# Kernel optimization log

Measured on AMD Instinct MI355X. Metric: run time of the kernel, lower is better.

The kernel has to match this reference:

```python
import jax, jax.numpy as jnp
import numpy as np

T = 4        # number of atom types (len(atomtype))
N = 65536    # number of atoms
D = 256      # nl[0] == nl[1] == nl[2]
EPS = 1e-5   # LayerNorm eps (torch default)


def setup_inputs() -> dict:
    key = jax.random.key(0)
    ks = jax.random.split(key, 16)
    s = 1.0 / np.sqrt(D)  # xavier-ish scale
    f32 = jnp.float32
    return {
        "density": jax.random.normal(ks[0], (N, D), f32),
        "species": jax.random.randint(ks[1], (N,), 0, T, jnp.int32),
        # first Linear(nl[0], nl[1]) per type
        "W0": jax.random.normal(ks[2], (T, D, D), f32) * s,
        "b0": jnp.zeros((T, D), f32),
        # ResBlock: actfun (Relu_like: alpha*silu(Wx+b)), LayerNorm, Linear
        "Wa": jax.random.normal(ks[3], (T, D, D), f32) * s,
        "ba": jnp.zeros((T, D), f32),
        "alpha_a": jnp.ones((T, D), f32),
        "gamma": jnp.ones((T, D), f32),
        "beta_ln": jnp.zeros((T, D), f32),
        "Wl": jax.random.normal(ks[4], (T, D, D), f32) * s,
        "bl": jnp.zeros((T, D), f32),
        # tail actfun(nl[nhid-1], nl[nhid])
        "Wf": jax.random.normal(ks[5], (T, D, D), f32) * s,
        "bf": jnp.zeros((T, D), f32),
        "alpha_f": jnp.ones((T, D), f32),
        # output Linear(nl[nhid], outputneuron=1); randomized (zero-init is degenerate for testing)
        "Wo": jax.random.normal(ks[6], (T, 1, D), f32) * s,
        "bo": jnp.zeros((T, 1), f32),
    }


def _layernorm(x, g, b):
    mu = jnp.mean(x, axis=-1, keepdims=True)
    var = jnp.mean((x - mu) ** 2, axis=-1, keepdims=True)
    return g * (x - mu) * jax.lax.rsqrt(var + EPS) + b


def _expert(W0, b0, Wa, ba, alpha_a, gamma, beta_ln, Wl, bl, Wf, bf, alpha_f, Wo, bo, density):
    # Sequential: Linear -> ResBlock(actfun, LN, Linear) -> actfun -> Linear
    x = density @ W0.T + b0                       # [N, D]
    h = alpha_a * jax.nn.silu(x @ Wa.T + ba)      # Relu_like actfun
    h = _layernorm(h, gamma, beta_ln)
    x = x + (h @ Wl.T + bl)                       # residual add
    x = alpha_f * jax.nn.silu(x @ Wf.T + bf)
    return x @ Wo.T + bo                          # [N, 1]


def reference(density, species, W0, b0, Wa, ba, alpha_a, gamma, beta_ln, Wl, bl, Wf, bf, alpha_f, Wo, bo):
    # Apply every type's expert to all atoms, then pick the row for each atom's type.
    # Same math as the torch gather/scatter dispatch (every species value is in [0, T)).
    y_all = jax.vmap(_expert, in_axes=(0,) * 14 + (None,))(
        W0, b0, Wa, ba, alpha_a, gamma, beta_ln, Wl, bl, Wf, bf, alpha_f, Wo, bo, density
    )  # [T, N, 1]
    return y_all[species, jnp.arange(N)]          # [N, 1]
```

## Files before the change

### kernel.cpp

```cpp
#include <hip/hip_runtime.h>
#include <hip/hip_bf16.h>


#define D 256
#define T 4
#define MT 64
#define NTHREADS 512
#define CSTRIDE 32

#define XSW(row, col) (((row) << 8) + ((col) ^ (((row) & 7) << 3)))

typedef __attribute__((ext_vector_type(8))) short bf16x8;
typedef __attribute__((ext_vector_type(4))) float f32x4;

__device__ __forceinline__ float bf2f(unsigned short s) {
    union { unsigned u; float f; } c;
    c.u = ((unsigned)s) << 16;
    return c.f;
}
__device__ __forceinline__ unsigned cvtpk(float a, float b) {
    unsigned r;
    asm("v_cvt_pk_bf16_f32 %0, %1, %2" : "=v"(r) : "v"(a), "v"(b));
    return r;
}
__device__ __forceinline__ float lo2f(unsigned u) { return bf2f((unsigned short)(u & 0xffffu)); }
__device__ __forceinline__ float hi2f(unsigned u) { return bf2f((unsigned short)(u >> 16)); }
__device__ __forceinline__ float silu(float v) {
    return v * __builtin_amdgcn_rcpf(1.f + __expf(-v));
}

extern "C" __global__ void k_prep(const int* __restrict__ species, int* cursors,
                                  int* __restrict__ perm, int N,
                                  const float* __restrict__ s0, const float* __restrict__ s1,
                                  const float* __restrict__ s2, const float* __restrict__ s3,
                                  unsigned short* __restrict__ d0, unsigned short* __restrict__ d1,
                                  unsigned short* __restrict__ d2, unsigned short* __restrict__ d3, int n4) {
    __shared__ int lh[T], lbase[T];
    int tid = threadIdx.x;
    if (tid < T) lh[tid] = 0;
    __syncthreads();
    int i = blockIdx.x * blockDim.x + tid;
    int t = -1, rank = 0;
    if (i < N) {
        t = species[i];
        rank = atomicAdd(&lh[t], 1);
    }
    if (i < n4) {
        float4 v;
        v = ((const float4*)s0)[i]; ((uint2*)d0)[i] = make_uint2(cvtpk(v.x, v.y), cvtpk(v.z, v.w));
        v = ((const float4*)s1)[i]; ((uint2*)d1)[i] = make_uint2(cvtpk(v.x, v.y), cvtpk(v.z, v.w));
        v = ((const float4*)s2)[i]; ((uint2*)d2)[i] = make_uint2(cvtpk(v.x, v.y), cvtpk(v.z, v.w));
        v = ((const float4*)s3)[i]; ((uint2*)d3)[i] = make_uint2(cvtpk(v.x, v.y), cvtpk(v.z, v.w));
    }
    __syncthreads();
    if (tid < T) lbase[tid] = atomicAdd(&cursors[tid * CSTRIDE], lh[tid]);
    __syncthreads();
    if (t >= 0) perm[t * N + lbase[t] + rank] = i;
}


extern "C" __global__ void __launch_bounds__(NTHREADS, 4)
fused_moe(const float* __restrict__ density,
          const int* __restrict__ perm,
          const int* __restrict__ counts,
          const unsigned short* __restrict__ W0b,
          const unsigned short* __restrict__ Wab,
          const unsigned short* __restrict__ Wlb,
          const unsigned short* __restrict__ Wfb,
          const float* __restrict__ b0g, const float* __restrict__ bag,
          const float* __restrict__ aag, const float* __restrict__ gg,
          const float* __restrict__ btg, const float* __restrict__ blg,
          const float* __restrict__ bfg, const float* __restrict__ afg,
          const float* __restrict__ Wog, const float* __restrict__ bog,
          float* __restrict__ out, int N)
{
    __shared__ unsigned short Xs[2][MT * D];
    __shared__ float Pb0[D], Pba[D], Paa[D], Pg[D], Pbt[D], Pbl[D], Pbf[D], Paf[D], Pwo[D];
    __shared__ float red1[NTHREADS], red2[NTHREADS];

    const int tid = threadIdx.x;

    int c[T];
#pragma unroll
    for (int i = 0; i < T; ++i) c[i] = counts[i * CSTRIDE];
    int t = -1, tile = 0, rem = blockIdx.x;
#pragma unroll
    for (int i = 0; i < T; ++i) {
        int ti = (c[i] + MT - 1) >> 6;
        if (t < 0) {
            if (rem < ti) { t = i; tile = rem; }
            else rem -= ti;
        }
    }
    if (t < 0) return;
    const int bstart = t * N + tile * MT;
    const int nrows = min(MT, c[t] - tile * MT);

    const int lane = tid & 63;
    const int w    = tid >> 6;
    const int ml   = lane & 15;
    const int qk   = (lane >> 4) * 8;
    const int qr   = (lane >> 4) * 4;

    const size_t wmat = (size_t)t * D * D;
    const unsigned short* W0t = W0b + wmat;
    const unsigned short* Wat = Wab + wmat;
    const unsigned short* Wlt = Wlb + wmat;
    const unsigned short* Wft = Wfb + wmat;

    bf16x8 pf0, pf1;
    auto prefA = [&](const unsigned short* __restrict__ W) {
        pf0 = *(const bf16x8*)(W + (size_t)(w * 32 + ml) * D + qk);
        pf1 = *(const bf16x8*)(W + (size_t)(w * 32 + 16 + ml) * D + qk);
    };

    prefA(W0t);

    if (tid < D) {
        int j = t * D + tid;
        Pb0[tid] = b0g[j]; Pba[tid] = bag[j]; Paa[tid] = aag[j];
        Pg[tid]  = gg[j];  Pbt[tid] = btg[j]; Pbl[tid] = blg[j];
        Pbf[tid] = bfg[j]; Paf[tid] = afg[j]; Pwo[tid] = Wog[j];
    }

#pragma unroll
    for (int p = 0; p < 2; ++p) {
        int row = p * 32 + (tid >> 4);
        int cbase = (tid & 15) * 4;
        if (row < nrows) {
            const float* src = density + (size_t)perm[bstart + row] * D;
#pragma unroll
            for (int j = 0; j < 4; ++j) {
                int col = cbase + j * 64;
                float4 v = *(const float4*)(src + col);
                *(uint2*)(&Xs[0][XSW(row, col)]) = make_uint2(cvtpk(v.x, v.y), cvtpk(v.z, v.w));
            }
        } else {
#pragma unroll
            for (int j = 0; j < 4; ++j)
                *(uint2*)(&Xs[0][XSW(row, cbase + j * 64)]) = make_uint2(0u, 0u);
        }
    }
    __syncthreads();

    f32x4 acc[2][4];
    const f32x4 zero4 = {0.f, 0.f, 0.f, 0.f};

    auto do_gemm = [&](const unsigned short* __restrict__ W, const unsigned short* __restrict__ Xb) {
#pragma unroll
        for (int mi = 0; mi < 2; ++mi)
#pragma unroll
            for (int ni = 0; ni < 4; ++ni) acc[mi][ni] = zero4;
#pragma unroll
        for (int k0 = 0; k0 < D; k0 += 32) {
            bf16x8 a[2], b[4];
            if (k0 == 0) { a[0] = pf0; a[1] = pf1; }
            else {
#pragma unroll
                for (int mi = 0; mi < 2; ++mi)
                    a[mi] = *(const bf16x8*)(W + (size_t)(w * 32 + mi * 16 + ml) * D + k0 + qk);
            }
#pragma unroll
            for (int ni = 0; ni < 4; ++ni)
                b[ni] = *(const bf16x8*)(Xb + XSW(ni * 16 + ml, k0 + qk));
#pragma unroll
            for (int mi = 0; mi < 2; ++mi)
#pragma unroll
                for (int ni = 0; ni < 4; ++ni)
                    acc[mi][ni] = __builtin_amdgcn_mfma_f32_16x16x32_bf16(a[mi], b[ni], acc[mi][ni], 0, 0, 0);
        }
    };


    do_gemm(W0t, Xs[0]);
    prefA(Wat);
    unsigned res[2][4][2];
#pragma unroll
    for (int mi = 0; mi < 2; ++mi) {
#pragma unroll
        for (int ni = 0; ni < 4; ++ni) {
            int r0 = w * 32 + mi * 16 + qr;
            int a0 = ni * 16 + ml;
            float4 bb = *(const float4*)(Pb0 + r0);
            unsigned p01 = cvtpk(acc[mi][ni][0] + bb.x, acc[mi][ni][1] + bb.y);
            unsigned p23 = cvtpk(acc[mi][ni][2] + bb.z, acc[mi][ni][3] + bb.w);
            res[mi][ni][0] = p01;
            res[mi][ni][1] = p23;
            *(uint2*)(&Xs[1][XSW(a0, r0)]) = make_uint2(p01, p23);
        }
    }
    __syncthreads();

    do_gemm(Wat, Xs[1]);
    prefA(Wlt);
#pragma unroll
    for (int mi = 0; mi < 2; ++mi) {
#pragma unroll
        for (int ni = 0; ni < 4; ++ni) {
            int r0 = w * 32 + mi * 16 + qr;
            int a0 = ni * 16 + ml;
            float4 bb = *(const float4*)(Pba + r0);
            float4 aa = *(const float4*)(Paa + r0);
            float v0 = aa.x * silu(acc[mi][ni][0] + bb.x);
            float v1 = aa.y * silu(acc[mi][ni][1] + bb.y);
            float v2 = aa.z * silu(acc[mi][ni][2] + bb.z);
            float v3 = aa.w * silu(acc[mi][ni][3] + bb.w);
            *(uint2*)(&Xs[0][XSW(a0, r0)]) = make_uint2(cvtpk(v0, v1), cvtpk(v2, v3));
        }
    }
    __syncthreads();

    {
        int row = tid & 63, q = tid >> 6;
        bf16x8 hv[4];
        float sum = 0.f, ssq = 0.f;
#pragma unroll
        for (int j = 0; j < 4; ++j) {
            hv[j] = *(const bf16x8*)(&Xs[0][XSW(row, q * 32 + j * 8)]);
#pragma unroll
            for (int e = 0; e < 8; ++e) {
                float f = bf2f((unsigned short)hv[j][e]);
                sum += f;
                ssq = fmaf(f, f, ssq);
            }
        }
        red1[tid] = sum; red2[tid] = ssq;
        __syncthreads();
        if (tid < MT) {
            float s = 0.f, sq = 0.f;
#pragma unroll
            for (int k = 0; k < 8; ++k) { s += red1[tid + 64 * k]; sq += red2[tid + 64 * k]; }
            float mu = s * (1.f / D);
            float var = sq * (1.f / D) - mu * mu;
            red1[tid] = mu;
            red2[tid] = rsqrtf(var + 1e-5f);
        }
        __syncthreads();
        float mu = red1[row], rs = red2[row];
#pragma unroll
        for (int j = 0; j < 4; ++j) {
            float n[8];
#pragma unroll
            for (int e = 0; e < 8; ++e) {
                int col = q * 32 + j * 8 + e;
                float f = bf2f((unsigned short)hv[j][e]);
                n[e] = fmaf((f - mu) * rs, Pg[col], Pbt[col]);
            }
            uint4 o = make_uint4(cvtpk(n[0], n[1]), cvtpk(n[2], n[3]),
                                 cvtpk(n[4], n[5]), cvtpk(n[6], n[7]));
            *(uint4*)(&Xs[1][XSW(row, q * 32 + j * 8)]) = o;
        }
    }
    __syncthreads();

    do_gemm(Wlt, Xs[1]);
    prefA(Wft);
#pragma unroll
    for (int mi = 0; mi < 2; ++mi) {
#pragma unroll
        for (int ni = 0; ni < 4; ++ni) {
            int r0 = w * 32 + mi * 16 + qr;
            int a0 = ni * 16 + ml;
            float4 bb = *(const float4*)(Pbl + r0);
            float v0 = acc[mi][ni][0] + bb.x + lo2f(res[mi][ni][0]);
            float v1 = acc[mi][ni][1] + bb.y + hi2f(res[mi][ni][0]);
            float v2 = acc[mi][ni][2] + bb.z + lo2f(res[mi][ni][1]);
            float v3 = acc[mi][ni][3] + bb.w + hi2f(res[mi][ni][1]);
            *(uint2*)(&Xs[0][XSW(a0, r0)]) = make_uint2(cvtpk(v0, v1), cvtpk(v2, v3));
        }
    }
    __syncthreads();

    do_gemm(Wft, Xs[0]);
#pragma unroll
    for (int mi = 0; mi < 2; ++mi) {
#pragma unroll
        for (int ni = 0; ni < 4; ++ni) {
            int r0 = w * 32 + mi * 16 + qr;
            int a0 = ni * 16 + ml;
            float4 bb = *(const float4*)(Pbf + r0);
            float4 aa = *(const float4*)(Paf + r0);
            float v0 = aa.x * silu(acc[mi][ni][0] + bb.x);
            float v1 = aa.y * silu(acc[mi][ni][1] + bb.y);
            float v2 = aa.z * silu(acc[mi][ni][2] + bb.z);
            float v3 = aa.w * silu(acc[mi][ni][3] + bb.w);
            *(uint2*)(&Xs[1][XSW(a0, r0)]) = make_uint2(cvtpk(v0, v1), cvtpk(v2, v3));
        }
    }
    __syncthreads();

    {
        int row = tid & 63, q = tid >> 6;
        float part = 0.f;
#pragma unroll
        for (int j = 0; j < 4; ++j) {
            bf16x8 hv = *(const bf16x8*)(&Xs[1][XSW(row, q * 32 + j * 8)]);
#pragma unroll
            for (int e = 0; e < 8; ++e)
                part = fmaf(bf2f((unsigned short)hv[e]), Pwo[q * 32 + j * 8 + e], part);
        }
        red1[tid] = part;
        __syncthreads();
        if (tid < nrows) {
            float val = bog[t];
#pragma unroll
            for (int k = 0; k < 8; ++k) val += red1[tid + 64 * k];
            out[perm[bstart + tid]] = val;
        }
    }
}


extern "C" void kernel_launch(void* const* d_in, const int* in_sizes, int n_in,
                              void* d_out, int out_size, void* d_ws, size_t ws_size,
                              hipStream_t stream) {
    const float* density = (const float*)d_in[0];
    const int*   species = (const int*)d_in[1];
    const float* W0      = (const float*)d_in[2];
    const float* b0      = (const float*)d_in[3];
    const float* Wa      = (const float*)d_in[4];
    const float* ba      = (const float*)d_in[5];
    const float* alpha_a = (const float*)d_in[6];
    const float* gamma   = (const float*)d_in[7];
    const float* beta_ln = (const float*)d_in[8];
    const float* Wl      = (const float*)d_in[9];
    const float* bl      = (const float*)d_in[10];
    const float* Wf      = (const float*)d_in[11];
    const float* bfv     = (const float*)d_in[12];
    const float* alpha_f = (const float*)d_in[13];
    const float* Wo      = (const float*)d_in[14];
    const float* bo      = (const float*)d_in[15];
    float* out = (float*)d_out;
    const int N = in_sizes[1];

    char* ws = (char*)d_ws;
    int* cursors = (int*)ws;
    int* perm    = (int*)(ws + 1024);
    const size_t wsz = (size_t)T * D * D;
    unsigned short* W0b = (unsigned short*)(ws + 1024 + (size_t)T * N * 4);
    unsigned short* Wab = W0b + wsz;
    unsigned short* Wlb = Wab + wsz;
    unsigned short* Wfb = Wlb + wsz;

    hipMemsetAsync(ws, 0, 512, stream);
    int n4 = (int)(wsz / 4);
    int pb = ((N > n4 ? N : n4) + 255) / 256;
    k_prep<<<pb, 256, 0, stream>>>(species, cursors, perm, N, W0, Wa, Wl, Wf,
                                   W0b, Wab, Wlb, Wfb, n4);

    int nblocks = (N + MT - 1) / MT + T;
    fused_moe<<<nblocks, NTHREADS, 0, stream>>>(density, perm, cursors, W0b, Wab, Wlb, Wfb,
                                                b0, ba, alpha_a, gamma, beta_ln, bl, bfv, alpha_f,
                                                Wo, bo, out, N);
}
```

Measured before the change: 199.0 us.

## Double-buffer weight fragment loads across k-steps and keep residual in LDS

The GEMM inner loop now prefetches the next 64-wide k-slab of weight fragments into a register double buffer while MFMAs run on the current slab, so global weight-load latency is hidden. The residual x, previously held in registers (res array), is now kept in a shared-memory buffer, and the LN output and later stages are rerouted to the other buffer. This lowers register pressure but adds more live A-fragment registers plus an extra LDS read per residual element.

```diff
diff --git a/kernel.cpp b/kernel.cpp
--- a/kernel.cpp
+++ b/kernel.cpp
@@ -108,10 +108,14 @@
     const unsigned short* Wlt = Wlb + wmat;
     const unsigned short* Wft = Wfb + wmat;
 
-    bf16x8 pf0, pf1;
+    bf16x8 abuf[2][4];
     auto prefA = [&](const unsigned short* __restrict__ W) {
-        pf0 = *(const bf16x8*)(W + (size_t)(w * 32 + ml) * D + qk);
-        pf1 = *(const bf16x8*)(W + (size_t)(w * 32 + 16 + ml) * D + qk);
+#pragma unroll
+        for (int s = 0; s < 2; ++s)
+#pragma unroll
+            for (int mi = 0; mi < 2; ++mi)
+                abuf[0][s * 2 + mi] =
+                    *(const bf16x8*)(W + (size_t)(w * 32 + mi * 16 + ml) * D + s * 32 + qk);
     };
 
     prefA(W0t);
@@ -152,29 +156,37 @@
 #pragma unroll
             for (int ni = 0; ni < 4; ++ni) acc[mi][ni] = zero4;
 #pragma unroll
-        for (int k0 = 0; k0 < D; k0 += 32) {
-            bf16x8 a[2], b[4];
-            if (k0 == 0) { a[0] = pf0; a[1] = pf1; }
-            else {
+        for (int kp = 0; kp < 4; ++kp) {
+            const int cur = kp & 1, nxt = cur ^ 1;
+            if (kp < 3) {
+                const int kb = (kp + 1) * 64;
+#pragma unroll
+                for (int s = 0; s < 2; ++s)
+#pragma unroll
+                    for (int mi = 0; mi < 2; ++mi)
+                        abuf[nxt][s * 2 + mi] =
+                            *(const bf16x8*)(W + (size_t)(w * 32 + mi * 16 + ml) * D + kb + s * 32 + qk);
+            }
+#pragma unroll
+            for (int s = 0; s < 2; ++s) {
+                const int k0 = kp * 64 + s * 32;
+                bf16x8 b[4];
+#pragma unroll
+                for (int ni = 0; ni < 4; ++ni)
+                    b[ni] = *(const bf16x8*)(Xb + XSW(ni * 16 + ml, k0 + qk));
 #pragma unroll
                 for (int mi = 0; mi < 2; ++mi)
-                    a[mi] = *(const bf16x8*)(W + (size_t)(w * 32 + mi * 16 + ml) * D + k0 + qk);
-            }
-#pragma unroll
-            for (int ni = 0; ni < 4; ++ni)
-                b[ni] = *(const bf16x8*)(Xb + XSW(ni * 16 + ml, k0 + qk));
-#pragma unroll
-            for (int mi = 0; mi < 2; ++mi)
-#pragma unroll
-                for (int ni = 0; ni < 4; ++ni)
-                    acc[mi][ni] = __builtin_amdgcn_mfma_f32_16x16x32_bf16(a[mi], b[ni], acc[mi][ni], 0, 0, 0);
+#pragma unroll
+                    for (int ni = 0; ni < 4; ++ni)
+                        acc[mi][ni] = __builtin_amdgcn_mfma_f32_16x16x32_bf16(
+                            abuf[cur][s * 2 + mi], b[ni], acc[mi][ni], 0, 0, 0);
+            }
         }
     };
 
 
     do_gemm(W0t, Xs[0]);
     prefA(Wat);
-    unsigned res[2][4][2];
 #pragma unroll
     for (int mi = 0; mi < 2; ++mi) {
 #pragma unroll
@@ -184,8 +196,6 @@
             float4 bb = *(const float4*)(Pb0 + r0);
             unsigned p01 = cvtpk(acc[mi][ni][0] + bb.x, acc[mi][ni][1] + bb.y);
             unsigned p23 = cvtpk(acc[mi][ni][2] + bb.z, acc[mi][ni][3] + bb.w);
-            res[mi][ni][0] = p01;
-            res[mi][ni][1] = p23;
             *(uint2*)(&Xs[1][XSW(a0, r0)]) = make_uint2(p01, p23);
         }
     }
@@ -248,12 +258,12 @@
             }
             uint4 o = make_uint4(cvtpk(n[0], n[1]), cvtpk(n[2], n[3]),
                                  cvtpk(n[4], n[5]), cvtpk(n[6], n[7]));
-            *(uint4*)(&Xs[1][XSW(row, q * 32 + j * 8)]) = o;
-        }
-    }
-    __syncthreads();
-
-    do_gemm(Wlt, Xs[1]);
+            *(uint4*)(&Xs[0][XSW(row, q * 32 + j * 8)]) = o;
+        }
+    }
+    __syncthreads();
+
+    do_gemm(Wlt, Xs[0]);
     prefA(Wft);
 #pragma unroll
     for (int mi = 0; mi < 2; ++mi) {
@@ -262,16 +272,17 @@
             int r0 = w * 32 + mi * 16 + qr;
             int a0 = ni * 16 + ml;
             float4 bb = *(const float4*)(Pbl + r0);
-            float v0 = acc[mi][ni][0] + bb.x + lo2f(res[mi][ni][0]);
-            float v1 = acc[mi][ni][1] + bb.y + hi2f(res[mi][ni][0]);
-            float v2 = acc[mi][ni][2] + bb.z + lo2f(res[mi][ni][1]);
-            float v3 = acc[mi][ni][3] + bb.w + hi2f(res[mi][ni][1]);
-            *(uint2*)(&Xs[0][XSW(a0, r0)]) = make_uint2(cvtpk(v0, v1), cvtpk(v2, v3));
-        }
-    }
-    __syncthreads();
-
-    do_gemm(Wft, Xs[0]);
+            uint2 old = *(const uint2*)(&Xs[1][XSW(a0, r0)]);
+            float v0 = acc[mi][ni][0] + bb.x + lo2f(old.x);
+            float v1 = acc[mi][ni][1] + bb.y + hi2f(old.x);
+            float v2 = acc[mi][ni][2] + bb.z + lo2f(old.y);
+            float v3 = acc[mi][ni][3] + bb.w + hi2f(old.y);
+            *(uint2*)(&Xs[1][XSW(a0, r0)]) = make_uint2(cvtpk(v0, v1), cvtpk(v2, v3));
+        }
+    }
+    __syncthreads();
+
+    do_gemm(Wft, Xs[1]);
 #pragma unroll
     for (int mi = 0; mi < 2; ++mi) {
 #pragma unroll
@@ -284,7 +295,7 @@
             float v1 = aa.y * silu(acc[mi][ni][1] + bb.y);
             float v2 = aa.z * silu(acc[mi][ni][2] + bb.z);
             float v3 = aa.w * silu(acc[mi][ni][3] + bb.w);
-            *(uint2*)(&Xs[1][XSW(a0, r0)]) = make_uint2(cvtpk(v0, v1), cvtpk(v2, v3));
+            *(uint2*)(&Xs[0][XSW(a0, r0)]) = make_uint2(cvtpk(v0, v1), cvtpk(v2, v3));
         }
     }
     __syncthreads();
@@ -294,7 +305,7 @@
         float part = 0.f;
 #pragma unroll
         for (int j = 0; j < 4; ++j) {
-            bf16x8 hv = *(const bf16x8*)(&Xs[1][XSW(row, q * 32 + j * 8)]);
+            bf16x8 hv = *(const bf16x8*)(&Xs[0][XSW(row, q * 32 + j * 8)]);
 #pragma unroll
             for (int e = 0; e < 8; ++e)
                 part = fmaf(bf2f((unsigned short)hv[e]), Pwo[q * 32 + j * 8 + e], part);
```

After: 199.3 us. No clear change (+0.2%).
